# Kernel optimization log

Hardware: AMD Instinct MI355X
Metric: run time of the kernel (lower is better)

The kernel has to match this reference:

```python
import jax, jax.numpy as jnp
import numpy as np

N_ITEM = 100000
DIV_TRADEOFF = 0.1


def setup_inputs() -> dict:
    key = jax.random.key(0)
    ks = jax.random.split(key, 9)
    B, K, L, D_LLM, H = 512, 8, 50, 768, 128
    return {
        "user_id": jax.random.randint(ks[0], (B,), 0, 50000),
        "base_model_preds": jax.random.randint(ks[1], (B, K, L), 0, N_ITEM + 1),
        "preference_in": jax.random.normal(ks[2], (B, H), jnp.float32),
        "pos_label": jax.random.normal(ks[3], (B, K), jnp.float32),
        "neg_label": jax.random.normal(ks[4], (B, K), jnp.float32),
        "user_embeddings": jax.random.normal(ks[5], (50000, H), jnp.float32) * 0.01,
        "item_embeddings": jax.random.normal(ks[6], (N_ITEM + 1, D_LLM), jnp.float32) * 0.02,
        "W_proj": jax.random.normal(ks[7], (D_LLM, H), jnp.float32) * (1.0 / np.sqrt(D_LLM)),
        "b_proj": jax.random.normal(ks[8], (H,), jnp.float32) * 0.01,
    }


def reference(user_id, base_model_preds, preference_in, pos_label, neg_label,
              user_embeddings, item_embeddings, W_proj, b_proj):
    B, K, L = base_model_preds.shape
    # masked gather-embed: ids outside (0, n_item] map to a zero row
    valid = (base_model_preds > 0) & (base_model_preds <= N_ITEM)
    safe_ids = jnp.where(valid, base_model_preds, 0)
    focus_llm = item_embeddings[safe_ids] * valid[..., None].astype(item_embeddings.dtype)  # [B,K,L,D_llm]
    # linear projection to hidden (bias applied everywhere, matching nn.Linear on zeroed rows)
    bm = jnp.einsum('bkld,dh->bklh', focus_llm, W_proj) + b_proj  # [B,K,L,H]
    # time-decay weighted sum over sequence positions
    time_w = 1.0 / jnp.log2(jnp.arange(L, dtype=jnp.float32) + 2.0)  # [L]
    basemodel_emb = jnp.einsum('bklh,l->bkh', bm, time_w)  # [B,K,H]
    # preference = DIEN(...) + user_emb  (DIEN output modeled by preference_in)
    preference = preference_in + user_embeddings[user_id]  # [B,H]
    wgts_org = jnp.einsum('bkh,bh->bk', basemodel_emb, preference)
    wgts = jax.nn.softmax(wgts_org, axis=-1)  # [B,K]
    pos_scores = jnp.sum(pos_label * wgts, axis=1)
    neg_scores = jnp.sum(neg_label * wgts, axis=1)
    loss = -jnp.sum(jax.nn.log_sigmoid(pos_scores - neg_scores))
    # diversity regularizer (use_div=True)
    cov_wgt = jax.lax.stop_gradient(wgts[:, None, :] + wgts[:, :, None])  # [B,K,K]
    cov_mask = 1.0 - jnp.eye(K, dtype=wgts.dtype)  # [K,K]
    gram = jnp.einsum('bih,bjh->bij', basemodel_emb, basemodel_emb) ** 2
    loss_div = DIV_TRADEOFF * jnp.mean(cov_mask[None] * gram * cov_wgt)
    return loss + loss_div
```

## Files before the change

### kernel.cpp

```cpp
#include <hip/hip_runtime.h>
#include <math.h>

#define B_SZ 512
#define K_SZ 8
#define L_SZ 50
#define DLLM 768
#define H_SZ 128
#define N_ITEM 100000
#define DIV_TRADEOFF 0.1f
#define M_PAD 100032

typedef float  f32x4 __attribute__((ext_vector_type(4)));
typedef short  bf16x8 __attribute__((ext_vector_type(8)));
typedef unsigned int u32x4 __attribute__((ext_vector_type(4)));
typedef unsigned short u16x8 __attribute__((ext_vector_type(8)));

__device__ __forceinline__ unsigned short f2bf(float f) {
    unsigned u = __float_as_uint(f);
    u += 0x7fffu + ((u >> 16) & 1u);
    return (unsigned short)(u >> 16);
}

__device__ __forceinline__ void gload_lds16(const void* g, void* l) {
    __builtin_amdgcn_global_load_lds(
        (const __attribute__((address_space(1))) unsigned*)g,
        (__attribute__((address_space(3))) unsigned*)l, 16, 0, 0);
}

__global__ __launch_bounds__(256) void k_wt(
    const float* __restrict__ W,
    unsigned short* __restrict__ Wt,
    float* __restrict__ out)
{
    __shared__ float tile[64][65];
    const int kb = blockIdx.x >> 1;
    const int nb = blockIdx.x & 1;
    const int t  = threadIdx.x;
    if (blockIdx.x == 0 && t == 0) out[0] = 0.0f;

    const int r  = t >> 2;
    const int c0 = (t & 3) * 16;
    #pragma unroll
    for (int j = 0; j < 4; ++j) {
        const float4 v = *(const float4*)(W + (size_t)(kb * 64 + r) * H_SZ + nb * 64 + c0 + j * 4);
        tile[r][c0 + j * 4 + 0] = v.x;
        tile[r][c0 + j * 4 + 1] = v.y;
        tile[r][c0 + j * 4 + 2] = v.z;
        tile[r][c0 + j * 4 + 3] = v.w;
    }
    __syncthreads();
    const int n  = t >> 2;
    const int k0 = (t & 3) * 16;
    u16x8 lo, hi;
    #pragma unroll
    for (int j = 0; j < 8; ++j) lo[j] = f2bf(tile[k0 + j][n]);
    #pragma unroll
    for (int j = 0; j < 8; ++j) hi[j] = f2bf(tile[k0 + 8 + j][n]);
    unsigned short* dst = Wt + (size_t)(nb * 64 + n) * DLLM + kb * 64 + k0;
    *(u16x8*)(dst)     = lo;
    *(u16x8*)(dst + 8) = hi;
}

__global__ __launch_bounds__(256) void k_proj(
    const float* __restrict__ item,
    const unsigned short* __restrict__ Wt,
    unsigned short* __restrict__ projb)
{
    __shared__ float          As[2][64 * 64];
    __shared__ unsigned short Bs[2][128 * 64];

    const int t    = threadIdx.x;
    const int brow = blockIdx.x * 64;
    const int w    = t >> 6;
    const int lane = t & 63;
    const int nl   = lane & 15;
    const int g    = lane >> 4;
    const int key  = nl & 7;

    const int a_rsub = (lane >> 4);
    const int a_gl   = lane & 15;
    const int b_nsub = (lane >> 3);
    const int b_gl   = lane & 7;
    const int b_key  = b_nsub & 7;

    const int r = w * 16 + nl;

    auto STAGE = [&](int d, int c) {
        const int kc = c * 64;
        #pragma unroll
        for (int i = 0; i < 4; ++i) {
            const int row_t = w * 16 + i * 4 + a_rsub;
            const int rowS  = (brow + row_t <= N_ITEM) ? (brow + row_t) : N_ITEM;
            const int ka    = (a_gl ^ (row_t & 7)) * 4;
            gload_lds16(item + (size_t)rowS * DLLM + kc + ka,
                        &As[d][w * 1024 + i * 256]);
        }
        #pragma unroll
        for (int i = 0; i < 4; ++i) {
            const int n_t = w * 32 + i * 8 + b_nsub;
            const int kb  = (b_gl ^ b_key) * 8;
            gload_lds16(Wt + (size_t)n_t * DLLM + kc + kb,
                        &Bs[d][w * 2048 + i * 512]);
        }
    };

    f32x4 acc[8];
    #pragma unroll
    for (int i = 0; i < 8; ++i) acc[i] = (f32x4){0.f, 0.f, 0.f, 0.f};

    STAGE(0, 0);

    for (int c = 0; c < 12; ++c) {
        const int cur = c & 1;
        if (c < 11) STAGE(cur ^ 1, c + 1);
        if (c < 11) asm volatile("s_waitcnt vmcnt(8)" ::: "memory");
        else        asm volatile("s_waitcnt vmcnt(0)" ::: "memory");
        __builtin_amdgcn_s_barrier();
        __builtin_amdgcn_sched_barrier(0);

        #pragma unroll
        for (int ks = 0; ks < 2; ++ks) {
            const f32x4 alo = *(const f32x4*)&As[cur][r * 64 + 4 * ((ks * 8 + 2 * g)     ^ key)];
            const f32x4 ahi = *(const f32x4*)&As[cur][r * 64 + 4 * ((ks * 8 + 2 * g + 1) ^ key)];
            unsigned p0, p1, p2, p3;
            asm("v_cvt_pk_bf16_f32 %0, %1, %2" : "=v"(p0) : "v"(alo.x), "v"(alo.y));
            asm("v_cvt_pk_bf16_f32 %0, %1, %2" : "=v"(p1) : "v"(alo.z), "v"(alo.w));
            asm("v_cvt_pk_bf16_f32 %0, %1, %2" : "=v"(p2) : "v"(ahi.x), "v"(ahi.y));
            asm("v_cvt_pk_bf16_f32 %0, %1, %2" : "=v"(p3) : "v"(ahi.z), "v"(ahi.w));
            union { u32x4 u; bf16x8 s; } af;
            af.u[0] = p0; af.u[1] = p1; af.u[2] = p2; af.u[3] = p3;

            #pragma unroll
            for (int nt = 0; nt < 8; ++nt) {
                const bf16x8 b = *(const bf16x8*)&Bs[cur][(nt * 16 + nl) * 64
                                                          + 8 * ((ks * 4 + g) ^ key)];
                acc[nt] = __builtin_amdgcn_mfma_f32_16x16x32_bf16(af.s, b, acc[nt], 0, 0, 0);
            }
        }
        asm volatile("s_waitcnt lgkmcnt(0)" ::: "memory");
        __builtin_amdgcn_s_barrier();
        __builtin_amdgcn_sched_barrier(0);
    }

    const int rbase = brow + w * 16 + 4 * g;
    #pragma unroll
    for (int nt = 0; nt < 8; ++nt) {
        #pragma unroll
        for (int rr = 0; rr < 4; ++rr) {
            projb[(size_t)(rbase + rr) * H_SZ + nt * 16 + nl] = f2bf(acc[nt][rr]);
        }
    }
}

__global__ __launch_bounds__(512) void k_gloss(
    const int* __restrict__ preds,
    const unsigned short* __restrict__ projb,
    const float* __restrict__ bproj,
    const int* __restrict__ user_id, const float* __restrict__ pref_in,
    const float* __restrict__ pos_label, const float* __restrict__ neg_label,
    const float* __restrict__ user_emb,
    float* __restrict__ out)
{
    const int b    = blockIdx.x;
    const int tid  = threadIdx.x;
    const int wv   = tid >> 6;
    const int lane = tid & 63;
    const int h2   = lane * 2;

    __shared__ float e[K_SZ][H_SZ + 1];
    __shared__ float pref[H_SZ];
    __shared__ float sdot[K_SZ];
    __shared__ float wg[K_SZ];
    __shared__ float lossb_s;

    {
        const int* __restrict__ p = preds + ((size_t)b * K_SZ + wv) * L_SZ;
        constexpr int PF = 8;
        unsigned buf[PF];
        float wgt[PF];
        #pragma unroll
        for (int i = 0; i < PF; ++i) {
            const int id = p[i];
            const bool v = (id > 0) && (id <= N_ITEM);
            wgt[i] = v ? (1.0f / log2f((float)(i + 2))) : 0.0f;
            buf[i] = *(const unsigned*)(projb + (size_t)(v ? id : 0) * H_SZ + h2);
        }
        float a0 = 0.f, a1 = 0.f;
        #pragma unroll
        for (int l = 0; l < L_SZ; ++l) {
            const int s = l % PF;
            const unsigned u = buf[s];
            const float w = wgt[s];
            if (l + PF < L_SZ) {
                const int id = p[l + PF];
                const bool v = (id > 0) && (id <= N_ITEM);
                wgt[s] = v ? (1.0f / log2f((float)(l + PF + 2))) : 0.0f;
                buf[s] = *(const unsigned*)(projb + (size_t)(v ? id : 0) * H_SZ + h2);
            }
            a0 += w * __uint_as_float(u << 16);
            a1 += w * __uint_as_float(u & 0xffff0000u);
        }
        float sumw = 0.f;
        #pragma unroll
        for (int l = 0; l < L_SZ; ++l) sumw += 1.0f / log2f((float)(l + 2));
        e[wv][h2]     = a0 + bproj[h2]     * sumw;
        e[wv][h2 + 1] = a1 + bproj[h2 + 1] * sumw;
    }
    if (tid < H_SZ) {
        const int uid = user_id[b];
        pref[tid] = pref_in[(size_t)b * H_SZ + tid] + user_emb[(size_t)uid * H_SZ + tid];
    }
    __syncthreads();

    if (tid < 256) {
        const int k = tid >> 5;
        const int l32 = tid & 31;
        float s = e[k][l32] * pref[l32] + e[k][l32 + 32] * pref[l32 + 32]
                + e[k][l32 + 64] * pref[l32 + 64] + e[k][l32 + 96] * pref[l32 + 96];
        #pragma unroll
        for (int m = 16; m >= 1; m >>= 1) s += __shfl_xor(s, m, 64);
        if (l32 == 0) sdot[k] = s;
    }
    __syncthreads();

    if (tid == 0) {
        float mx = sdot[0];
        #pragma unroll
        for (int k = 1; k < K_SZ; ++k) mx = fmaxf(mx, sdot[k]);
        float sum = 0.f; float ex[K_SZ];
        #pragma unroll
        for (int k = 0; k < K_SZ; ++k) { ex[k] = expf(sdot[k] - mx); sum += ex[k]; }
        float ps = 0.f, ns = 0.f;
        #pragma unroll
        for (int k = 0; k < K_SZ; ++k) {
            const float w = ex[k] / sum;
            wg[k] = w;
            ps += pos_label[(size_t)b * K_SZ + k] * w;
            ns += neg_label[(size_t)b * K_SZ + k] * w;
        }
        const float x = ps - ns;
        lossb_s = fmaxf(-x, 0.f) + log1pf(expf(-fabsf(x)));
    }
    __syncthreads();

    if (tid < 64) {
        const int i = tid >> 3;
        const int j = tid & 7;
        float gsum = 0.f;
        for (int h = 0; h < H_SZ; ++h) gsum += e[i][h] * e[j][h];
        float v = (i != j) ? (gsum * gsum * (wg[i] + wg[j])) : 0.f;
        #pragma unroll
        for (int m = 32; m >= 1; m >>= 1) v += __shfl_xor(v, m, 64);
        if (tid == 0) {
            const float mean_div = v / (float)(B_SZ * K_SZ * K_SZ);
            atomicAdd(out, lossb_s + DIV_TRADEOFF * mean_div);
        }
    }
}

__global__ __launch_bounds__(192) void k_gather_fb(
    const int* __restrict__ preds, const float* __restrict__ item,
    float* __restrict__ wf, float* __restrict__ out)
{
    const int bk  = blockIdx.x;
    const int tid = threadIdx.x;
    if (bk == 0 && tid == 0) out[0] = 0.0f;
    const int* __restrict__ p = preds + (size_t)bk * L_SZ;
    const float* __restrict__ ibase = item + (size_t)tid * 4;
    float4 acc = make_float4(0.f, 0.f, 0.f, 0.f);
    constexpr int PF = 8;
    float4 buf[PF]; float wgt[PF];
    #pragma unroll
    for (int i = 0; i < PF; ++i) {
        const int id = p[i];
        const bool v = (id > 0) && (id <= N_ITEM);
        wgt[i] = v ? (1.0f / log2f((float)(i + 2))) : 0.0f;
        buf[i] = *(const float4*)(ibase + (size_t)(v ? id : 0) * DLLM);
    }
    #pragma unroll
    for (int l = 0; l < L_SZ; ++l) {
        const int s = l % PF;
        const float4 v4 = buf[s];
        const float  w  = wgt[s];
        if (l + PF < L_SZ) {
            const int id = p[l + PF];
            const bool v = (id > 0) && (id <= N_ITEM);
            wgt[s] = v ? (1.0f / log2f((float)(l + PF + 2))) : 0.0f;
            buf[s] = *(const float4*)(ibase + (size_t)(v ? id : 0) * DLLM);
        }
        acc.x += w * v4.x; acc.y += w * v4.y; acc.z += w * v4.z; acc.w += w * v4.w;
    }
    *(float4*)(wf + (size_t)bk * DLLM + (size_t)tid * 4) = acc;
}

__global__ __launch_bounds__(256) void k_projloss_fb(
    const float* __restrict__ wf, const float* __restrict__ W,
    const float* __restrict__ bproj, const int* __restrict__ user_id,
    const float* __restrict__ pref_in, const float* __restrict__ pos_label,
    const float* __restrict__ neg_label, const float* __restrict__ user_emb,
    float* __restrict__ out)
{
    const int b   = blockIdx.x;
    const int tid = threadIdx.x;
    const int c   = tid & (H_SZ - 1);
    const int rg  = tid >> 7;
    __shared__ float A[K_SZ][H_SZ];
    __shared__ float e[K_SZ][H_SZ + 1];
    __shared__ float pref[H_SZ];
    __shared__ float sdot[K_SZ];
    __shared__ float wg[K_SZ];
    __shared__ float lossb_s;
    float acc[4] = {0.f, 0.f, 0.f, 0.f};
    const size_t rowbase = (size_t)b * K_SZ;
    for (int kb = 0; kb < DLLM; kb += H_SZ) {
        __syncthreads();
        {
            const int r  = tid >> 5;
            const int kk = (tid & 31) * 4;
            *(float4*)&A[r][kk] = *(const float4*)(wf + (rowbase + r) * DLLM + kb + kk);
        }
        __syncthreads();
        #pragma unroll 4
        for (int k = 0; k < H_SZ; k += 4) {
            const float4 a0 = *(const float4*)&A[rg][k];
            const float4 a1 = *(const float4*)&A[rg + 2][k];
            const float4 a2 = *(const float4*)&A[rg + 4][k];
            const float4 a3 = *(const float4*)&A[rg + 6][k];
            const float* Wp = W + (size_t)(kb + k) * H_SZ + c;
            const float w0 = Wp[0]; const float w1 = Wp[H_SZ];
            const float w2 = Wp[2 * H_SZ]; const float w3 = Wp[3 * H_SZ];
            acc[0] += a0.x * w0 + a0.y * w1 + a0.z * w2 + a0.w * w3;
            acc[1] += a1.x * w0 + a1.y * w1 + a1.z * w2 + a1.w * w3;
            acc[2] += a2.x * w0 + a2.y * w1 + a2.z * w2 + a2.w * w3;
            acc[3] += a3.x * w0 + a3.y * w1 + a3.z * w2 + a3.w * w3;
        }
    }
    float sumw = 0.f;
    #pragma unroll
    for (int l = 0; l < L_SZ; ++l) sumw += 1.0f / log2f((float)(l + 2));
    const float bterm = bproj[c] * sumw;
    #pragma unroll
    for (int ri = 0; ri < 4; ++ri) e[rg + 2 * ri][c] = acc[ri] + bterm;
    if (tid < H_SZ) {
        const int uid = user_id[b];
        pref[tid] = pref_in[(size_t)b * H_SZ + tid] + user_emb[(size_t)uid * H_SZ + tid];
    }
    __syncthreads();
    {
        const int k    = tid >> 5;
        const int lane = tid & 31;
        float s = e[k][lane] * pref[lane] + e[k][lane + 32] * pref[lane + 32]
                + e[k][lane + 64] * pref[lane + 64] + e[k][lane + 96] * pref[lane + 96];
        #pragma unroll
        for (int m = 16; m >= 1; m >>= 1) s += __shfl_xor(s, m, 64);
        if (lane == 0) sdot[k] = s;
    }
    __syncthreads();
    if (tid == 0) {
        float mx = sdot[0];
        #pragma unroll
        for (int k = 1; k < K_SZ; ++k) mx = fmaxf(mx, sdot[k]);
        float sum = 0.f; float ex[K_SZ];
        #pragma unroll
        for (int k = 0; k < K_SZ; ++k) { ex[k] = expf(sdot[k] - mx); sum += ex[k]; }
        float ps = 0.f, ns = 0.f;
        #pragma unroll
        for (int k = 0; k < K_SZ; ++k) {
            const float w = ex[k] / sum;
            wg[k] = w;
            ps += pos_label[(size_t)b * K_SZ + k] * w;
            ns += neg_label[(size_t)b * K_SZ + k] * w;
        }
        const float x = ps - ns;
        lossb_s = fmaxf(-x, 0.f) + log1pf(expf(-fabsf(x)));
    }
    __syncthreads();
    if (tid < 64) {
        const int i = tid >> 3;
        const int j = tid & 7;
        float g = 0.f;
        for (int h = 0; h < H_SZ; ++h) g += e[i][h] * e[j][h];
        float v = (i != j) ? (g * g * (wg[i] + wg[j])) : 0.f;
        #pragma unroll
        for (int m = 32; m >= 1; m >>= 1) v += __shfl_xor(v, m, 64);
        if (tid == 0) {
            const float mean_div = v / (float)(B_SZ * K_SZ * K_SZ);
            atomicAdd(out, lossb_s + DIV_TRADEOFF * mean_div);
        }
    }
}

extern "C" void kernel_launch(void* const* d_in, const int* in_sizes, int n_in,
                              void* d_out, int out_size, void* d_ws, size_t ws_size,
                              hipStream_t stream) {
    const int*   user_id   = (const int*)  d_in[0];
    const int*   preds     = (const int*)  d_in[1];
    const float* pref_in   = (const float*)d_in[2];
    const float* pos_label = (const float*)d_in[3];
    const float* neg_label = (const float*)d_in[4];
    const float* user_emb  = (const float*)d_in[5];
    const float* item_emb  = (const float*)d_in[6];
    const float* W_proj    = (const float*)d_in[7];
    const float* b_proj    = (const float*)d_in[8];

    float* out = (float*)d_out;

    const size_t projb_bytes = (size_t)M_PAD * H_SZ * sizeof(unsigned short);
    const size_t wt_off      = projb_bytes;
    const size_t wt_bytes    = (size_t)H_SZ * DLLM * sizeof(unsigned short);
    const size_t need        = wt_off + wt_bytes;

    if (ws_size >= need) {
        unsigned short* projb = (unsigned short*)d_ws;
        unsigned short* Wt    = (unsigned short*)((char*)d_ws + wt_off);

        k_wt<<<24, 256, 0, stream>>>(W_proj, Wt, out);
        k_proj<<<M_PAD / 64, 256, 0, stream>>>(item_emb, Wt, projb);
        k_gloss<<<B_SZ, 512, 0, stream>>>(preds, projb, b_proj, user_id, pref_in,
                                          pos_label, neg_label, user_emb, out);
    } else {
        float* wf = (float*)d_ws;
        k_gather_fb<<<B_SZ * K_SZ, 192, 0, stream>>>(preds, item_emb, wf, out);
        k_projloss_fb<<<B_SZ, 256, 0, stream>>>(wf, W_proj, b_proj, user_id, pref_in,
                                                pos_label, neg_label, user_emb, out);
    }
}
```

Measured before the change: 104.4 us.

## Preload full A tile as bf16 in LDS and triple-buffer W tiles

The projection GEMM kernel now loads each block's 64 item rows entirely up front through registers, converts them to bf16 once and stores them swizzled in LDS (96KB), instead of streaming fp32 A chunks with async LDS loads per k-step. The W operand moves to a three-stage buffer with a deeper prefetch. This drops the per-iteration A conversion and halves A's LDS footprint per element, but LDS use rises to about 144KB, which cuts occupancy and serialises the A load before any MFMA work starts.

```diff
diff --git a/kernel.cpp b/kernel.cpp
--- a/kernel.cpp
+++ b/kernel.cpp
@@ -66,8 +66,8 @@
     const unsigned short* __restrict__ Wt,
     unsigned short* __restrict__ projb)
 {
-    __shared__ float          As[2][64 * 64];
-    __shared__ unsigned short Bs[2][128 * 64];
+    __shared__ unsigned short As16[64 * DLLM];
+    __shared__ unsigned short Bs[3][128 * 64];
 
     const int t    = threadIdx.x;
     const int brow = blockIdx.x * 64;
@@ -77,24 +77,14 @@
     const int g    = lane >> 4;
     const int key  = nl & 7;
 
-    const int a_rsub = (lane >> 4);
-    const int a_gl   = lane & 15;
     const int b_nsub = (lane >> 3);
     const int b_gl   = lane & 7;
     const int b_key  = b_nsub & 7;
 
     const int r = w * 16 + nl;
 
-    auto STAGE = [&](int d, int c) {
+    auto STAGE_B = [&](int d, int c) {
         const int kc = c * 64;
-        #pragma unroll
-        for (int i = 0; i < 4; ++i) {
-            const int row_t = w * 16 + i * 4 + a_rsub;
-            const int rowS  = (brow + row_t <= N_ITEM) ? (brow + row_t) : N_ITEM;
-            const int ka    = (a_gl ^ (row_t & 7)) * 4;
-            gload_lds16(item + (size_t)rowS * DLLM + kc + ka,
-                        &As[d][w * 1024 + i * 256]);
-        }
         #pragma unroll
         for (int i = 0; i < 4; ++i) {
             const int n_t = w * 32 + i * 8 + b_nsub;
@@ -104,37 +94,60 @@
         }
     };
 
+    STAGE_B(0, 0);
+    STAGE_B(1, 1);
+
+    {
+        const int prow  = t >> 2;
+        const int psub  = t & 3;
+        const int prowS = (brow + prow <= N_ITEM) ? (brow + prow) : N_ITEM;
+        const float* __restrict__ psrc = item + (size_t)prowS * DLLM + psub * 192;
+        char* As_b = (char*)As16;
+        const int pkey = prow & 7;
+
+        #pragma unroll
+        for (int bi = 0; bi < 4; ++bi) {
+            f32x4 L[12];
+            #pragma unroll
+            for (int jj = 0; jj < 12; ++jj)
+                L[jj] = *(const f32x4*)(psrc + (bi * 12 + jj) * 4);
+            #pragma unroll
+            for (int jj = 0; jj < 12; ++jj) {
+                const int j = bi * 12 + jj;
+                unsigned p0, p1;
+                asm("v_cvt_pk_bf16_f32 %0, %1, %2" : "=v"(p0) : "v"(L[jj].x), "v"(L[jj].y));
+                asm("v_cvt_pk_bf16_f32 %0, %1, %2" : "=v"(p1) : "v"(L[jj].z), "v"(L[jj].w));
+                const int q = psub * 24 + (j >> 1);
+                const int h = j & 1;
+                uint2 d; d.x = p0; d.y = p1;
+                *(uint2*)(As_b + prow * 1536 + ((q ^ pkey) << 4) + h * 8) = d;
+            }
+        }
+    }
+    __syncthreads();
+
     f32x4 acc[8];
     #pragma unroll
     for (int i = 0; i < 8; ++i) acc[i] = (f32x4){0.f, 0.f, 0.f, 0.f};
 
-    STAGE(0, 0);
-
     for (int c = 0; c < 12; ++c) {
-        const int cur = c & 1;
-        if (c < 11) STAGE(cur ^ 1, c + 1);
-        if (c < 11) asm volatile("s_waitcnt vmcnt(8)" ::: "memory");
-        else        asm volatile("s_waitcnt vmcnt(0)" ::: "memory");
+        const int cur = c % 3;
+        if (c < 10) STAGE_B((c + 2) % 3, c + 2);
+        if      (c < 10) asm volatile("s_waitcnt vmcnt(8)" ::: "memory");
+        else if (c == 10) asm volatile("s_waitcnt vmcnt(4)" ::: "memory");
+        else              asm volatile("s_waitcnt vmcnt(0)" ::: "memory");
         __builtin_amdgcn_s_barrier();
         __builtin_amdgcn_sched_barrier(0);
 
         #pragma unroll
         for (int ks = 0; ks < 2; ++ks) {
-            const f32x4 alo = *(const f32x4*)&As[cur][r * 64 + 4 * ((ks * 8 + 2 * g)     ^ key)];
-            const f32x4 ahi = *(const f32x4*)&As[cur][r * 64 + 4 * ((ks * 8 + 2 * g + 1) ^ key)];
-            unsigned p0, p1, p2, p3;
-            asm("v_cvt_pk_bf16_f32 %0, %1, %2" : "=v"(p0) : "v"(alo.x), "v"(alo.y));
-            asm("v_cvt_pk_bf16_f32 %0, %1, %2" : "=v"(p1) : "v"(alo.z), "v"(alo.w));
-            asm("v_cvt_pk_bf16_f32 %0, %1, %2" : "=v"(p2) : "v"(ahi.x), "v"(ahi.y));
-            asm("v_cvt_pk_bf16_f32 %0, %1, %2" : "=v"(p3) : "v"(ahi.z), "v"(ahi.w));
-            union { u32x4 u; bf16x8 s; } af;
-            af.u[0] = p0; af.u[1] = p1; af.u[2] = p2; af.u[3] = p3;
-
+            const bf16x8 af = *(const bf16x8*)&As16[r * DLLM
+                                + (((c * 8 + ks * 4 + g) ^ key) << 3)];
             #pragma unroll
             for (int nt = 0; nt < 8; ++nt) {
                 const bf16x8 b = *(const bf16x8*)&Bs[cur][(nt * 16 + nl) * 64
                                                           + 8 * ((ks * 4 + g) ^ key)];
-                acc[nt] = __builtin_amdgcn_mfma_f32_16x16x32_bf16(af.s, b, acc[nt], 0, 0, 0);
+                acc[nt] = __builtin_amdgcn_mfma_f32_16x16x32_bf16(af, b, acc[nt], 0, 0, 0);
             }
         }
         asm volatile("s_waitcnt lgkmcnt(0)" ::: "memory");
```

New measurement: 173.9 us. 1.67x slower.

## Stage item rows through registers as bf16 and triple-buffer W tiles in k_proj

Applied to the files above, without the earlier changes.

The projection GEMM now loads the fp32 item-embedding tile into registers, converts it to bf16 once, and writes the packed bf16 into a swizzled LDS buffer, instead of DMA-ing fp32 straight to LDS and converting inside every MFMA step. The W tile moves from double to triple buffering, prefetched two chunks ahead, and the loop drops one barrier per iteration. The aim is to halve LDS footprint and read traffic for A, take conversion out of the MFMA inner loop, and hide more global latency. The cost is extra VGPRs for the register staging and fragile hand-counted vmcnt waits.

```diff
diff --git a/kernel.cpp b/kernel.cpp
--- a/kernel.cpp
+++ b/kernel.cpp
@@ -66,8 +66,8 @@
     const unsigned short* __restrict__ Wt,
     unsigned short* __restrict__ projb)
 {
-    __shared__ float          As[2][64 * 64];
-    __shared__ unsigned short Bs[2][128 * 64];
+    __shared__ unsigned short As[2][64 * 64];
+    __shared__ unsigned short Bs[3][128 * 64];
 
     const int t    = threadIdx.x;
     const int brow = blockIdx.x * 64;
@@ -76,25 +76,13 @@
     const int nl   = lane & 15;
     const int g    = lane >> 4;
     const int key  = nl & 7;
-
-    const int a_rsub = (lane >> 4);
-    const int a_gl   = lane & 15;
+    const int r    = w * 16 + nl;
+
     const int b_nsub = (lane >> 3);
     const int b_gl   = lane & 7;
     const int b_key  = b_nsub & 7;
-
-    const int r = w * 16 + nl;
-
-    auto STAGE = [&](int d, int c) {
+    auto STAGE_B = [&](int d, int c) {
         const int kc = c * 64;
-        #pragma unroll
-        for (int i = 0; i < 4; ++i) {
-            const int row_t = w * 16 + i * 4 + a_rsub;
-            const int rowS  = (brow + row_t <= N_ITEM) ? (brow + row_t) : N_ITEM;
-            const int ka    = (a_gl ^ (row_t & 7)) * 4;
-            gload_lds16(item + (size_t)rowS * DLLM + kc + ka,
-                        &As[d][w * 1024 + i * 256]);
-        }
         #pragma unroll
         for (int i = 0; i < 4; ++i) {
             const int n_t = w * 32 + i * 8 + b_nsub;
@@ -104,42 +92,76 @@
         }
     };
 
+    const int ar    = t >> 2;
+    const int aseg  = t & 3;
+    const int akey  = ar & 7;
+    const int arowS = (brow + ar <= N_ITEM) ? (brow + ar) : N_ITEM;
+    const float* __restrict__ asrc = item + (size_t)arowS * DLLM + aseg * 16;
+
+    f32x4 La[4];
+    auto A_ISSUE = [&](int c) {
+        const float* p = asrc + c * 64;
+        #pragma unroll
+        for (int j = 0; j < 4; ++j) La[j] = *(const f32x4*)(p + j * 4);
+    };
+    auto A_WRITE = [&](int d) {
+        unsigned p0, p1, p2, p3, p4, p5, p6, p7;
+        asm("v_cvt_pk_bf16_f32 %0, %1, %2" : "=v"(p0) : "v"(La[0].x), "v"(La[0].y));
+        asm("v_cvt_pk_bf16_f32 %0, %1, %2" : "=v"(p1) : "v"(La[0].z), "v"(La[0].w));
+        asm("v_cvt_pk_bf16_f32 %0, %1, %2" : "=v"(p2) : "v"(La[1].x), "v"(La[1].y));
+        asm("v_cvt_pk_bf16_f32 %0, %1, %2" : "=v"(p3) : "v"(La[1].z), "v"(La[1].w));
+        asm("v_cvt_pk_bf16_f32 %0, %1, %2" : "=v"(p4) : "v"(La[2].x), "v"(La[2].y));
+        asm("v_cvt_pk_bf16_f32 %0, %1, %2" : "=v"(p5) : "v"(La[2].z), "v"(La[2].w));
+        asm("v_cvt_pk_bf16_f32 %0, %1, %2" : "=v"(p6) : "v"(La[3].x), "v"(La[3].y));
+        asm("v_cvt_pk_bf16_f32 %0, %1, %2" : "=v"(p7) : "v"(La[3].z), "v"(La[3].w));
+        u32x4 d0; d0[0] = p0; d0[1] = p1; d0[2] = p2; d0[3] = p3;
+        u32x4 d1; d1[0] = p4; d1[1] = p5; d1[2] = p6; d1[3] = p7;
+        char* base = (char*)&As[d][0] + ar * 128;
+        *(u32x4*)(base + (((aseg * 2    ) ^ akey) << 4)) = d0;
+        *(u32x4*)(base + (((aseg * 2 + 1) ^ akey) << 4)) = d1;
+    };
+
     f32x4 acc[8];
     #pragma unroll
     for (int i = 0; i < 8; ++i) acc[i] = (f32x4){0.f, 0.f, 0.f, 0.f};
 
-    STAGE(0, 0);
+    A_ISSUE(0);
+    STAGE_B(0, 0);
+    STAGE_B(1, 1);
+    asm volatile("s_waitcnt vmcnt(8)" ::: "memory");
+    __builtin_amdgcn_sched_barrier(0);
+    A_WRITE(0);
+    asm volatile("s_waitcnt vmcnt(4) lgkmcnt(0)" ::: "memory");
+    __builtin_amdgcn_s_barrier();
+    __builtin_amdgcn_sched_barrier(0);
 
     for (int c = 0; c < 12; ++c) {
-        const int cur = c & 1;
-        if (c < 11) STAGE(cur ^ 1, c + 1);
-        if (c < 11) asm volatile("s_waitcnt vmcnt(8)" ::: "memory");
-        else        asm volatile("s_waitcnt vmcnt(0)" ::: "memory");
-        __builtin_amdgcn_s_barrier();
+        if (c < 11) A_ISSUE(c + 1);
+        if (c < 10) STAGE_B((c + 2) % 3, c + 2);
         __builtin_amdgcn_sched_barrier(0);
 
+        const unsigned short* Asc = &As[c & 1][0];
+        const unsigned short* Bsc = &Bs[c % 3][0];
         #pragma unroll
         for (int ks = 0; ks < 2; ++ks) {
-            const f32x4 alo = *(const f32x4*)&As[cur][r * 64 + 4 * ((ks * 8 + 2 * g)     ^ key)];
-            const f32x4 ahi = *(const f32x4*)&As[cur][r * 64 + 4 * ((ks * 8 + 2 * g + 1) ^ key)];
-            unsigned p0, p1, p2, p3;
-            asm("v_cvt_pk_bf16_f32 %0, %1, %2" : "=v"(p0) : "v"(alo.x), "v"(alo.y));
-            asm("v_cvt_pk_bf16_f32 %0, %1, %2" : "=v"(p1) : "v"(alo.z), "v"(alo.w));
-            asm("v_cvt_pk_bf16_f32 %0, %1, %2" : "=v"(p2) : "v"(ahi.x), "v"(ahi.y));
-            asm("v_cvt_pk_bf16_f32 %0, %1, %2" : "=v"(p3) : "v"(ahi.z), "v"(ahi.w));
-            union { u32x4 u; bf16x8 s; } af;
-            af.u[0] = p0; af.u[1] = p1; af.u[2] = p2; af.u[3] = p3;
-
+            const int q = (ks * 4 + g) ^ key;
+            const bf16x8 af = *(const bf16x8*)((const char*)Asc + r * 128 + (q << 4));
             #pragma unroll
             for (int nt = 0; nt < 8; ++nt) {
-                const bf16x8 b = *(const bf16x8*)&Bs[cur][(nt * 16 + nl) * 64
-                                                          + 8 * ((ks * 4 + g) ^ key)];
-                acc[nt] = __builtin_amdgcn_mfma_f32_16x16x32_bf16(af.s, b, acc[nt], 0, 0, 0);
+                const bf16x8 b = *(const bf16x8*)&Bsc[(nt * 16 + nl) * 64 + 8 * q];
+                acc[nt] = __builtin_amdgcn_mfma_f32_16x16x32_bf16(af, b, acc[nt], 0, 0, 0);
             }
         }
-        asm volatile("s_waitcnt lgkmcnt(0)" ::: "memory");
-        __builtin_amdgcn_s_barrier();
-        __builtin_amdgcn_sched_barrier(0);
+
+        if (c < 11) {
+            if (c < 10) asm volatile("s_waitcnt vmcnt(4)" ::: "memory");
+            else        asm volatile("s_waitcnt vmcnt(0)" ::: "memory");
+            __builtin_amdgcn_sched_barrier(0);
+            A_WRITE((c + 1) & 1);
+            asm volatile("s_waitcnt lgkmcnt(0)" ::: "memory");
+            __builtin_amdgcn_s_barrier();
+            __builtin_amdgcn_sched_barrier(0);
+        }
     }
 
     const int rbase = brow + w * 16 + 4 * g;
```

Measured after the change: 106.7 us. 1.02x slower.

## Give each wave private LDS staging to drop block barriers in projection GEMM

Applied to the files above, without the earlier changes.

Each wave in the projection kernel now stages its own 16 item rows and its own full copy of the W tile into a private LDS region, in K chunks of 32 instead of 64. This removes both s_barrier calls per iteration, so the four waves no longer wait on each other. In exchange, every wave loads the whole W chunk, which quadruples W traffic through global/L2 and LDS. The loop also runs twice as many shorter iterations and uses a new swizzle for B.

```diff
diff --git a/kernel.cpp b/kernel.cpp
--- a/kernel.cpp
+++ b/kernel.cpp
@@ -66,41 +66,37 @@
     const unsigned short* __restrict__ Wt,
     unsigned short* __restrict__ projb)
 {
-    __shared__ float          As[2][64 * 64];
-    __shared__ unsigned short Bs[2][128 * 64];
+    __shared__ float          As[2][4][16 * 32];
+    __shared__ unsigned short Bs[2][4][128 * 32];
 
     const int t    = threadIdx.x;
-    const int brow = blockIdx.x * 64;
     const int w    = t >> 6;
     const int lane = t & 63;
     const int nl   = lane & 15;
     const int g    = lane >> 4;
-    const int key  = nl & 7;
-
-    const int a_rsub = (lane >> 4);
-    const int a_gl   = lane & 15;
-    const int b_nsub = (lane >> 3);
-    const int b_gl   = lane & 7;
-    const int b_key  = b_nsub & 7;
-
-    const int r = w * 16 + nl;
+    const int wrow = blockIdx.x * 64 + w * 16;
+
+    const int a_rt = lane >> 3;
+    const int a_gr = lane & 7;
+    const int b_nt = lane >> 2;
+    const int b_gr = lane & 3;
 
     auto STAGE = [&](int d, int c) {
-        const int kc = c * 64;
-        #pragma unroll
-        for (int i = 0; i < 4; ++i) {
-            const int row_t = w * 16 + i * 4 + a_rsub;
-            const int rowS  = (brow + row_t <= N_ITEM) ? (brow + row_t) : N_ITEM;
-            const int ka    = (a_gl ^ (row_t & 7)) * 4;
-            gload_lds16(item + (size_t)rowS * DLLM + kc + ka,
-                        &As[d][w * 1024 + i * 256]);
-        }
-        #pragma unroll
-        for (int i = 0; i < 4; ++i) {
-            const int n_t = w * 32 + i * 8 + b_nsub;
-            const int kb  = (b_gl ^ b_key) * 8;
-            gload_lds16(Wt + (size_t)n_t * DLLM + kc + kb,
-                        &Bs[d][w * 2048 + i * 512]);
+        const int kc = c * 32;
+        #pragma unroll
+        for (int i = 0; i < 2; ++i) {
+            const int rt = i * 8 + a_rt;
+            const int rg = wrow + rt;
+            const int rs = (rg <= N_ITEM) ? rg : N_ITEM;
+            gload_lds16(item + (size_t)rs * DLLM + kc + (a_gr ^ (rt & 7)) * 4,
+                        &As[d][w][i * 256]);
+        }
+        #pragma unroll
+        for (int i = 0; i < 8; ++i) {
+            const int nt_ = i * 16 + b_nt;
+            const int kb  = (b_gr ^ ((nt_ ^ (nt_ >> 2)) & 3)) * 8;
+            gload_lds16(Wt + (size_t)nt_ * DLLM + kc + kb,
+                        &Bs[d][w][i * 512]);
         }
     };
 
@@ -110,39 +106,39 @@
 
     STAGE(0, 0);
 
-    for (int c = 0; c < 12; ++c) {
-        const int cur = c & 1;
-        if (c < 11) STAGE(cur ^ 1, c + 1);
-        if (c < 11) asm volatile("s_waitcnt vmcnt(8)" ::: "memory");
-        else        asm volatile("s_waitcnt vmcnt(0)" ::: "memory");
-        __builtin_amdgcn_s_barrier();
+    const int key = nl & 7;
+    for (int c = 0; c < 24; ++c) {
+        if (c + 1 < 24) {
+            STAGE((c + 1) & 1, c + 1);
+            asm volatile("s_waitcnt vmcnt(10)" ::: "memory");
+        } else {
+            asm volatile("s_waitcnt vmcnt(0)" ::: "memory");
+        }
         __builtin_amdgcn_sched_barrier(0);
 
-        #pragma unroll
-        for (int ks = 0; ks < 2; ++ks) {
-            const f32x4 alo = *(const f32x4*)&As[cur][r * 64 + 4 * ((ks * 8 + 2 * g)     ^ key)];
-            const f32x4 ahi = *(const f32x4*)&As[cur][r * 64 + 4 * ((ks * 8 + 2 * g + 1) ^ key)];
-            unsigned p0, p1, p2, p3;
-            asm("v_cvt_pk_bf16_f32 %0, %1, %2" : "=v"(p0) : "v"(alo.x), "v"(alo.y));
-            asm("v_cvt_pk_bf16_f32 %0, %1, %2" : "=v"(p1) : "v"(alo.z), "v"(alo.w));
-            asm("v_cvt_pk_bf16_f32 %0, %1, %2" : "=v"(p2) : "v"(ahi.x), "v"(ahi.y));
-            asm("v_cvt_pk_bf16_f32 %0, %1, %2" : "=v"(p3) : "v"(ahi.z), "v"(ahi.w));
-            union { u32x4 u; bf16x8 s; } af;
-            af.u[0] = p0; af.u[1] = p1; af.u[2] = p2; af.u[3] = p3;
-
-            #pragma unroll
-            for (int nt = 0; nt < 8; ++nt) {
-                const bf16x8 b = *(const bf16x8*)&Bs[cur][(nt * 16 + nl) * 64
-                                                          + 8 * ((ks * 4 + g) ^ key)];
-                acc[nt] = __builtin_amdgcn_mfma_f32_16x16x32_bf16(af.s, b, acc[nt], 0, 0, 0);
-            }
-        }
-        asm volatile("s_waitcnt lgkmcnt(0)" ::: "memory");
-        __builtin_amdgcn_s_barrier();
-        __builtin_amdgcn_sched_barrier(0);
-    }
-
-    const int rbase = brow + w * 16 + 4 * g;
+        const float*          Ap = &As[c & 1][w][0];
+        const unsigned short* Bp = &Bs[c & 1][w][0];
+
+        const f32x4 alo = *(const f32x4*)(Ap + nl * 32 + ((2 * g)     ^ key) * 4);
+        const f32x4 ahi = *(const f32x4*)(Ap + nl * 32 + ((2 * g + 1) ^ key) * 4);
+        unsigned p0, p1, p2, p3;
+        asm("v_cvt_pk_bf16_f32 %0, %1, %2" : "=v"(p0) : "v"(alo.x), "v"(alo.y));
+        asm("v_cvt_pk_bf16_f32 %0, %1, %2" : "=v"(p1) : "v"(alo.z), "v"(alo.w));
+        asm("v_cvt_pk_bf16_f32 %0, %1, %2" : "=v"(p2) : "v"(ahi.x), "v"(ahi.y));
+        asm("v_cvt_pk_bf16_f32 %0, %1, %2" : "=v"(p3) : "v"(ahi.z), "v"(ahi.w));
+        union { u32x4 u; bf16x8 s; } af;
+        af.u[0] = p0; af.u[1] = p1; af.u[2] = p2; af.u[3] = p3;
+
+        #pragma unroll
+        for (int nt = 0; nt < 8; ++nt) {
+            const int m  = nt * 16 + nl;
+            const int bq = (g ^ ((m ^ (m >> 2)) & 3)) * 8;
+            const bf16x8 b = *(const bf16x8*)(Bp + m * 32 + bq);
+            acc[nt] = __builtin_amdgcn_mfma_f32_16x16x32_bf16(af.s, b, acc[nt], 0, 0, 0);
+        }
+    }
+
+    const int rbase = wrow + 4 * g;
     #pragma unroll
     for (int nt = 0; nt < 8; ++nt) {
         #pragma unroll
```

Result: slower. 172.6 us (+65.4%).
